# Kernel tuning notes

Measured on AMD Instinct MI355X. Metric: run time of the kernel, lower is better.

The kernel has to match this reference:

```python
import jax, jax.numpy as jnp
import numpy as np

N, K, C_IN, C = 64, 64, 128, 128


def setup_inputs() -> dict:
    key = jax.random.key(0)
    ks = jax.random.split(key, 12)
    s_in = 1.0 / np.sqrt(C_IN + 1)
    s_c = 1.0 / np.sqrt(C)
    s_2c = 1.0 / np.sqrt(2 * C)
    return {
        "t": jax.random.uniform(ks[0], (1,), dtype=jnp.float32),
        "x": jax.random.normal(ks[1], (N, K, C_IN), dtype=jnp.float32),
        # ConcatLinear: Linear(C_IN + 1, C) applied to cat([x, t], -1)
        "W_lin": jax.random.normal(ks[2], (C, C_IN + 1), dtype=jnp.float32) * s_in,
        "b_lin": jax.random.normal(ks[3], (C,), dtype=jnp.float32) * s_in,
        # unary_passing: Linear(C,C) -> tanh -> Linear(C,C)
        "Wu1": jax.random.normal(ks[4], (C, C), dtype=jnp.float32) * s_c,
        "bu1": jax.random.normal(ks[5], (C,), dtype=jnp.float32) * s_c,
        "Wu2": jax.random.normal(ks[6], (C, C), dtype=jnp.float32) * s_c,
        "bu2": jax.random.normal(ks[7], (C,), dtype=jnp.float32) * s_c,
        # binary_passing: Linear(2C,C) -> tanh -> Linear(C,C)
        "Wb1": jax.random.normal(ks[8], (C, 2 * C), dtype=jnp.float32) * s_2c,
        "bb1": jax.random.normal(ks[9], (C,), dtype=jnp.float32) * s_2c,
        "Wb2": jax.random.normal(ks[10], (C, C), dtype=jnp.float32) * s_c,
        "bb2": jax.random.normal(ks[11], (C,), dtype=jnp.float32) * s_c,
    }


def reference(t, x, W_lin, b_lin, Wu1, bu1, Wu2, bu2, Wb1, bb1, Wb2, bb2):
    n, k, _ = x.shape
    # linear_map: ConcatLinear(t, x) = Linear(cat([x, t*ones], -1))
    tt = jnp.broadcast_to(t.reshape(1, 1, 1), (n, k, 1)).astype(x.dtype)
    h = jnp.concatenate([x, tt], axis=-1) @ W_lin.T + b_lin  # [N,K,C]

    # unary message
    unary = jnp.tanh(h @ Wu1.T + bu1) @ Wu2.T + bu2  # [N,K,C]

    # binary message. h_matrix[n,i,j] = cat([h[n,j], h[n,i]]); split Wb1 into
    # the halves acting on each part to avoid materializing the 2C concat.
    A = h @ Wb1[:, :C].T          # contribution of h[n,j], [N,K,C]
    B = h @ Wb1[:, C:].T          # contribution of h[n,i], [N,K,C]
    pre = A[:, None, :, :] + B[:, :, None, :] + bb1       # [N,i,j,C]
    msg = jnp.tanh(pre) @ Wb2.T + bb2                     # [N,i,j,C]

    # fully-connected graph: E[i,j] = 1 - eye (E is None, masks is None)
    E = 1.0 - jnp.eye(k, dtype=x.dtype)                   # [i,j]
    msg = msg * E[None, :, :, None]
    denom = 1.0 + jnp.sum(E, axis=0)                      # per-j, [K]
    binary = jnp.sum(msg, axis=1) / denom[None, :, None]  # [N,K,C]

    return unary + binary
```

## Files before the change

kernel.cpp:

```cpp
#include <hip/hip_runtime.h>

#define LS 132
#define USTR 20
#define ROW_ELEMS 524288
#define EXPC 2.8853900817779268f

__device__ __forceinline__ float sigterm(float x) {
    float e = __builtin_amdgcn_exp2f(x * EXPC);
    return __builtin_amdgcn_rcpf(e + 1.0f);
}
__device__ __forceinline__ float tanh_fast(float x) {
    return 1.0f - 2.0f * sigterm(x);
}

__device__ __forceinline__ void stage64(const float* __restrict__ X, int r0,
                                        float* __restrict__ xs, int tid) {
    const float4* src = reinterpret_cast<const float4*>(X + (size_t)r0 * 128);
#pragma unroll
    for (int p = 0; p < 8; ++p) {
        const int q = p * 256 + tid;
        const int r = q >> 5;
        const int k4 = (q & 31) << 2;
        *reinterpret_cast<float4*>(&xs[r * LS + k4]) = src[q];
    }
}

template <int NC>
__device__ __forceinline__ void accum_lds(const float* __restrict__ xs,
                                          const float* __restrict__ wt,
                                          int lane, int wc0,
                                          float (&acc)[NC]) {
#pragma unroll 8
    for (int kq = 0; kq < 32; ++kq) {
        const float4 a =
            *reinterpret_cast<const float4*>(&xs[lane * LS + kq * 4]);
#pragma unroll
        for (int c = 0; c < NC; ++c) {
            const float4 w = *reinterpret_cast<const float4*>(
                &wt[(wc0 + c) * 128 + kq * 4]);
            acc[c] = fmaf(a.x, w.x, acc[c]);
            acc[c] = fmaf(a.y, w.y, acc[c]);
            acc[c] = fmaf(a.z, w.z, acc[c]);
            acc[c] = fmaf(a.w, w.w, acc[c]);
        }
    }
}

__global__ __launch_bounds__(256) void k1_h(const float* __restrict__ x,
                                            const float* __restrict__ W_lin,
                                            const float* __restrict__ b_lin,
                                            const float* __restrict__ tp,
                                            float* __restrict__ h) {
    __shared__ float xs[64 * LS];
    const int tid = threadIdx.x;
    const int lane = tid & 63;
    const int wv = __builtin_amdgcn_readfirstlane(tid >> 6);
    const int r0 = blockIdx.x * 64;
    const int c0 = blockIdx.y * 8 + wv * 2;
    stage64(x, r0, xs, tid);
    __syncthreads();
    float acc[2] = {0.f, 0.f};
    const float* w0 = W_lin + (c0 + 0) * 129;
    const float* w1 = W_lin + (c0 + 1) * 129;
#pragma unroll 8
    for (int kq = 0; kq < 32; ++kq) {
        const float4 a =
            *reinterpret_cast<const float4*>(&xs[lane * LS + kq * 4]);
        acc[0] = fmaf(a.x, w0[kq * 4 + 0], acc[0]);
        acc[0] = fmaf(a.y, w0[kq * 4 + 1], acc[0]);
        acc[0] = fmaf(a.z, w0[kq * 4 + 2], acc[0]);
        acc[0] = fmaf(a.w, w0[kq * 4 + 3], acc[0]);
        acc[1] = fmaf(a.x, w1[kq * 4 + 0], acc[1]);
        acc[1] = fmaf(a.y, w1[kq * 4 + 1], acc[1]);
        acc[1] = fmaf(a.z, w1[kq * 4 + 2], acc[1]);
        acc[1] = fmaf(a.w, w1[kq * 4 + 3], acc[1]);
    }
    const float tv = tp[0];
    float2 o;
    o.x = acc[0] + b_lin[c0 + 0] + tv * W_lin[(c0 + 0) * 129 + 128];
    o.y = acc[1] + b_lin[c0 + 1] + tv * W_lin[(c0 + 1) * 129 + 128];
    *reinterpret_cast<float2*>(&h[(size_t)(r0 + lane) * 128 + c0]) = o;
}

__global__ __launch_bounds__(256) void k2_fused(
    const float* __restrict__ h, const float* __restrict__ Wu1,
    const float* __restrict__ bu1, const float* __restrict__ Wb1,
    const float* __restrict__ bb1, float* __restrict__ T,
    float* __restrict__ S) {
    __shared__ float smem[64 * LS + 32 * 128];
    float* xs = smem;
    float* wt = smem + 64 * LS;
    float* us = smem;
    float* vs = smem + 64 * USTR;
    const int tid = threadIdx.x;
    const int lane = tid & 63;
    const int wv = __builtin_amdgcn_readfirstlane(tid >> 6);
    const int r0 = blockIdx.x * 64;
    const int j = blockIdx.y;
    stage64(h, r0, xs, tid);
    {
        const int cb = j < 8 ? j * 16 : 0;
        const int cg0 = j >= 8 ? (j - 8) * 32 : 0;
#pragma unroll
        for (int p = 0; p < 4; ++p) {
            const int q = p * 256 + tid;
            const int row = q >> 5;
            const int k4 = (q & 31) << 2;
            const float* src;
            if (j < 8)
                src = (row < 16) ? (Wb1 + (cb + row) * 256 + k4)
                                 : (Wb1 + (cb + row - 16) * 256 + 128 + k4);
            else
                src = Wu1 + (cg0 + row) * 128 + k4;
            *reinterpret_cast<float4*>(&wt[row * 128 + k4]) =
                *reinterpret_cast<const float4*>(src);
        }
    }
    __syncthreads();

    if (j < 8) {
        const int cb = j * 16;
        const bool isB = wv >= 2;
        const int half = wv & 1;
        const int c0 = cb + half * 8;
        const int wc0 = (isB ? 16 : 0) + half * 8;
        float acc[8] = {0.f, 0.f, 0.f, 0.f, 0.f, 0.f, 0.f, 0.f};
        accum_lds<8>(xs, wt, lane, wc0, acc);
        float e[8];
#pragma unroll
        for (int c = 0; c < 8; ++c) {
            const float v = isB ? (acc[c] + bb1[c0 + c]) : acc[c];
            e[c] = __builtin_amdgcn_exp2f(v * EXPC);
        }
        __syncthreads();
        float* dstl = (isB ? vs : us) + lane * USTR + half * 8;
        *reinterpret_cast<float4*>(dstl) = make_float4(e[0], e[1], e[2], e[3]);
        *reinterpret_cast<float4*>(dstl + 4) =
            make_float4(e[4], e[5], e[6], e[7]);
        __syncthreads();

        const int lc = wv * 4;
        const float4 u =
            *reinterpret_cast<const float4*>(&us[lane * USTR + lc]);
        float s0 = 0.f, s1 = 0.f, s2 = 0.f, s3 = 0.f;
#pragma unroll 8
        for (int i = 0; i < 64; ++i) {
            const float4 v =
                *reinterpret_cast<const float4*>(&vs[i * USTR + lc]);
            s0 += __builtin_amdgcn_rcpf(fmaf(u.x, v.x, 1.0f));
            s1 += __builtin_amdgcn_rcpf(fmaf(u.y, v.y, 1.0f));
            s2 += __builtin_amdgcn_rcpf(fmaf(u.z, v.z, 1.0f));
            s3 += __builtin_amdgcn_rcpf(fmaf(u.w, v.w, 1.0f));
        }
        const float4 vj =
            *reinterpret_cast<const float4*>(&vs[lane * USTR + lc]);
        float4 o;
        o.x = (63.0f - 2.0f * (s0 - __builtin_amdgcn_rcpf(fmaf(u.x, vj.x, 1.0f)))) * 0.015625f;
        o.y = (63.0f - 2.0f * (s1 - __builtin_amdgcn_rcpf(fmaf(u.y, vj.y, 1.0f)))) * 0.015625f;
        o.z = (63.0f - 2.0f * (s2 - __builtin_amdgcn_rcpf(fmaf(u.z, vj.z, 1.0f)))) * 0.015625f;
        o.w = (63.0f - 2.0f * (s3 - __builtin_amdgcn_rcpf(fmaf(u.w, vj.w, 1.0f)))) * 0.015625f;
        *reinterpret_cast<float4*>(&S[(size_t)(r0 + lane) * 128 + cb + lc]) = o;
    } else {
        const int c0 = (j - 8) * 32 + wv * 8;
        float acc[8] = {0.f, 0.f, 0.f, 0.f, 0.f, 0.f, 0.f, 0.f};
        accum_lds<8>(xs, wt, lane, wv * 8, acc);
        float4 v0, v1;
        v0.x = tanh_fast(acc[0] + bu1[c0 + 0]);
        v0.y = tanh_fast(acc[1] + bu1[c0 + 1]);
        v0.z = tanh_fast(acc[2] + bu1[c0 + 2]);
        v0.w = tanh_fast(acc[3] + bu1[c0 + 3]);
        v1.x = tanh_fast(acc[4] + bu1[c0 + 4]);
        v1.y = tanh_fast(acc[5] + bu1[c0 + 5]);
        v1.z = tanh_fast(acc[6] + bu1[c0 + 6]);
        v1.w = tanh_fast(acc[7] + bu1[c0 + 7]);
        float* dst = T + (size_t)(r0 + lane) * 128 + c0;
        *reinterpret_cast<float4*>(dst) = v0;
        *reinterpret_cast<float4*>(dst + 4) = v1;
    }
}

__global__ __launch_bounds__(256) void k4_out(
    const float* __restrict__ T, const float* __restrict__ S,
    const float* __restrict__ Wu2, const float* __restrict__ Wb2,
    const float* __restrict__ bu2, const float* __restrict__ bb2,
    float* __restrict__ out) {
    __shared__ float xs[64 * LS];
    const int tid = threadIdx.x;
    const int lane = tid & 63;
    const int wv = __builtin_amdgcn_readfirstlane(tid >> 6);
    const int r0 = blockIdx.x * 64;
    const int c0 = blockIdx.y * 8 + wv * 2;
    stage64(T, r0, xs, tid);
    __syncthreads();
    float acc[2] = {0.f, 0.f};
    {
        const float* w0 = Wu2 + (c0 + 0) * 128;
        const float* w1 = Wu2 + (c0 + 1) * 128;
#pragma unroll 8
        for (int kq = 0; kq < 32; ++kq) {
            const float4 a =
                *reinterpret_cast<const float4*>(&xs[lane * LS + kq * 4]);
            acc[0] = fmaf(a.x, w0[kq * 4 + 0], acc[0]);
            acc[0] = fmaf(a.y, w0[kq * 4 + 1], acc[0]);
            acc[0] = fmaf(a.z, w0[kq * 4 + 2], acc[0]);
            acc[0] = fmaf(a.w, w0[kq * 4 + 3], acc[0]);
            acc[1] = fmaf(a.x, w1[kq * 4 + 0], acc[1]);
            acc[1] = fmaf(a.y, w1[kq * 4 + 1], acc[1]);
            acc[1] = fmaf(a.z, w1[kq * 4 + 2], acc[1]);
            acc[1] = fmaf(a.w, w1[kq * 4 + 3], acc[1]);
        }
    }
    __syncthreads();
    stage64(S, r0, xs, tid);
    __syncthreads();
    {
        const float* w0 = Wb2 + (c0 + 0) * 128;
        const float* w1 = Wb2 + (c0 + 1) * 128;
#pragma unroll 8
        for (int kq = 0; kq < 32; ++kq) {
            const float4 a =
                *reinterpret_cast<const float4*>(&xs[lane * LS + kq * 4]);
            acc[0] = fmaf(a.x, w0[kq * 4 + 0], acc[0]);
            acc[0] = fmaf(a.y, w0[kq * 4 + 1], acc[0]);
            acc[0] = fmaf(a.z, w0[kq * 4 + 2], acc[0]);
            acc[0] = fmaf(a.w, w0[kq * 4 + 3], acc[0]);
            acc[1] = fmaf(a.x, w1[kq * 4 + 0], acc[1]);
            acc[1] = fmaf(a.y, w1[kq * 4 + 1], acc[1]);
            acc[1] = fmaf(a.z, w1[kq * 4 + 2], acc[1]);
            acc[1] = fmaf(a.w, w1[kq * 4 + 3], acc[1]);
        }
    }
    float2 o;
    o.x = acc[0] + bu2[c0 + 0] + 0.984375f * bb2[c0 + 0];
    o.y = acc[1] + bu2[c0 + 1] + 0.984375f * bb2[c0 + 1];
    *reinterpret_cast<float2*>(&out[(size_t)(r0 + lane) * 128 + c0]) = o;
}

extern "C" void kernel_launch(void* const* d_in, const int* in_sizes, int n_in,
                              void* d_out, int out_size, void* d_ws,
                              size_t ws_size, hipStream_t stream) {
    const float* t = (const float*)d_in[0];
    const float* x = (const float*)d_in[1];
    const float* W_lin = (const float*)d_in[2];
    const float* b_lin = (const float*)d_in[3];
    const float* Wu1 = (const float*)d_in[4];
    const float* bu1 = (const float*)d_in[5];
    const float* Wu2 = (const float*)d_in[6];
    const float* bu2 = (const float*)d_in[7];
    const float* Wb1 = (const float*)d_in[8];
    const float* bb1 = (const float*)d_in[9];
    const float* Wb2 = (const float*)d_in[10];
    const float* bb2 = (const float*)d_in[11];
    float* out = (float*)d_out;

    float* ws = (float*)d_ws;
    float* h = ws;
    float* T = ws + 1 * ROW_ELEMS;
    float* S = ws + 2 * ROW_ELEMS;

    k1_h<<<dim3(64, 16), 256, 0, stream>>>(x, W_lin, b_lin, t, h);
    k2_fused<<<dim3(64, 12), 256, 0, stream>>>(h, Wu1, bu1, Wb1, bb1, T, S);
    k4_out<<<dim3(64, 16), 256, 0, stream>>>(T, S, Wu2, Wb2, bu2, bb2, out);
    (void)in_sizes; (void)n_in; (void)out_size; (void)ws_size;
}
```

Before: 32.80 us.

## Merge three kernels into one persistent megakernel with per-group atomic counters

Replaces the three launches (h projection, fused first layers, output layers) with one 64x12-block kernel. Blocks coordinate through per-row-group atomic counters with release/acquire spin-waits, so later stages start as soon as their rows are ready. The next stage's weights are staged into LDS before waiting. This removes two launch gaps and kernel-boundary drains, but adds a memset launch and spin-wait overhead. It also relies on all dependent blocks being co-resident to avoid deadlock.

```diff
diff --git a/kernel.cpp b/kernel.cpp
--- a/kernel.cpp
+++ b/kernel.cpp
@@ -5,12 +5,9 @@
 #define ROW_ELEMS 524288
 #define EXPC 2.8853900817779268f
 
-__device__ __forceinline__ float sigterm(float x) {
+__device__ __forceinline__ float tanh_fast(float x) {
     float e = __builtin_amdgcn_exp2f(x * EXPC);
-    return __builtin_amdgcn_rcpf(e + 1.0f);
-}
-__device__ __forceinline__ float tanh_fast(float x) {
-    return 1.0f - 2.0f * sigterm(x);
+    return 1.0f - 2.0f * __builtin_amdgcn_rcpf(e + 1.0f);
 }
 
 __device__ __forceinline__ void stage64(const float* __restrict__ X, int r0,
@@ -46,47 +43,15 @@
     }
 }
 
-__global__ __launch_bounds__(256) void k1_h(const float* __restrict__ x,
-                                            const float* __restrict__ W_lin,
-                                            const float* __restrict__ b_lin,
-                                            const float* __restrict__ tp,
-                                            float* __restrict__ h) {
-    __shared__ float xs[64 * LS];
-    const int tid = threadIdx.x;
-    const int lane = tid & 63;
-    const int wv = __builtin_amdgcn_readfirstlane(tid >> 6);
-    const int r0 = blockIdx.x * 64;
-    const int c0 = blockIdx.y * 8 + wv * 2;
-    stage64(x, r0, xs, tid);
-    __syncthreads();
-    float acc[2] = {0.f, 0.f};
-    const float* w0 = W_lin + (c0 + 0) * 129;
-    const float* w1 = W_lin + (c0 + 1) * 129;
-#pragma unroll 8
-    for (int kq = 0; kq < 32; ++kq) {
-        const float4 a =
-            *reinterpret_cast<const float4*>(&xs[lane * LS + kq * 4]);
-        acc[0] = fmaf(a.x, w0[kq * 4 + 0], acc[0]);
-        acc[0] = fmaf(a.y, w0[kq * 4 + 1], acc[0]);
-        acc[0] = fmaf(a.z, w0[kq * 4 + 2], acc[0]);
-        acc[0] = fmaf(a.w, w0[kq * 4 + 3], acc[0]);
-        acc[1] = fmaf(a.x, w1[kq * 4 + 0], acc[1]);
-        acc[1] = fmaf(a.y, w1[kq * 4 + 1], acc[1]);
-        acc[1] = fmaf(a.z, w1[kq * 4 + 2], acc[1]);
-        acc[1] = fmaf(a.w, w1[kq * 4 + 3], acc[1]);
-    }
-    const float tv = tp[0];
-    float2 o;
-    o.x = acc[0] + b_lin[c0 + 0] + tv * W_lin[(c0 + 0) * 129 + 128];
-    o.y = acc[1] + b_lin[c0 + 1] + tv * W_lin[(c0 + 1) * 129 + 128];
-    *reinterpret_cast<float2*>(&h[(size_t)(r0 + lane) * 128 + c0]) = o;
-}
-
-__global__ __launch_bounds__(256) void k2_fused(
-    const float* __restrict__ h, const float* __restrict__ Wu1,
-    const float* __restrict__ bu1, const float* __restrict__ Wb1,
-    const float* __restrict__ bb1, float* __restrict__ T,
-    float* __restrict__ S) {
+__global__ __launch_bounds__(256) void megakernel(
+    const float* __restrict__ tp, const float* __restrict__ x,
+    const float* __restrict__ W_lin, const float* __restrict__ b_lin,
+    const float* __restrict__ Wu1, const float* __restrict__ bu1,
+    const float* __restrict__ Wu2, const float* __restrict__ bu2,
+    const float* __restrict__ Wb1, const float* __restrict__ bb1,
+    const float* __restrict__ Wb2, const float* __restrict__ bb2,
+    float* __restrict__ h, float* __restrict__ T, float* __restrict__ S,
+    float* __restrict__ out, unsigned int* __restrict__ cnt) {
     __shared__ float smem[64 * LS + 32 * 128];
     float* xs = smem;
     float* wt = smem + 64 * LS;
@@ -95,9 +60,38 @@
     const int tid = threadIdx.x;
     const int lane = tid & 63;
     const int wv = __builtin_amdgcn_readfirstlane(tid >> 6);
-    const int r0 = blockIdx.x * 64;
+    const int g = blockIdx.x;
     const int j = blockIdx.y;
-    stage64(h, r0, xs, tid);
+    const int r0 = g * 64;
+    unsigned int* c1 = cnt + g;
+    unsigned int* c2 = cnt + 64 + g;
+
+    if (j < 8) {
+        stage64(x, r0, xs, tid);
+#pragma unroll
+        for (int p = 0; p < 8; ++p) {
+            const int q = p * 256 + tid;
+            const int row = q >> 7;
+            const int col = q & 127;
+            wt[row * 128 + col] = W_lin[(j * 16 + row) * 129 + col];
+        }
+        __syncthreads();
+        float acc[4] = {0.f, 0.f, 0.f, 0.f};
+        accum_lds<4>(xs, wt, lane, wv * 4, acc);
+        const int c0 = j * 16 + wv * 4;
+        const float tv = tp[0];
+        float4 o;
+        o.x = acc[0] + b_lin[c0 + 0] + tv * W_lin[(c0 + 0) * 129 + 128];
+        o.y = acc[1] + b_lin[c0 + 1] + tv * W_lin[(c0 + 1) * 129 + 128];
+        o.z = acc[2] + b_lin[c0 + 2] + tv * W_lin[(c0 + 2) * 129 + 128];
+        o.w = acc[3] + b_lin[c0 + 3] + tv * W_lin[(c0 + 3) * 129 + 128];
+        *reinterpret_cast<float4*>(&h[(size_t)(r0 + lane) * 128 + c0]) = o;
+        __syncthreads();
+        if (tid == 0)
+            __hip_atomic_fetch_add(c1, 1u, __ATOMIC_RELEASE,
+                                   __HIP_MEMORY_SCOPE_AGENT);
+    }
+
     {
         const int cb = j < 8 ? j * 16 : 0;
         const int cg0 = j >= 8 ? (j - 8) * 32 : 0;
@@ -116,6 +110,13 @@
                 *reinterpret_cast<const float4*>(src);
         }
     }
+    if (tid == 0) {
+        while (__hip_atomic_load(c1, __ATOMIC_ACQUIRE,
+                                 __HIP_MEMORY_SCOPE_AGENT) < 8u)
+            __builtin_amdgcn_s_sleep(1);
+    }
+    __syncthreads();
+    stage64(h, r0, xs, tid);
     __syncthreads();
 
     if (j < 8) {
@@ -177,63 +178,46 @@
         *reinterpret_cast<float4*>(dst) = v0;
         *reinterpret_cast<float4*>(dst + 4) = v1;
     }
-}
-
-__global__ __launch_bounds__(256) void k4_out(
-    const float* __restrict__ T, const float* __restrict__ S,
-    const float* __restrict__ Wu2, const float* __restrict__ Wb2,
-    const float* __restrict__ bu2, const float* __restrict__ bb2,
-    float* __restrict__ out) {
-    __shared__ float xs[64 * LS];
-    const int tid = threadIdx.x;
-    const int lane = tid & 63;
-    const int wv = __builtin_amdgcn_readfirstlane(tid >> 6);
-    const int r0 = blockIdx.x * 64;
-    const int c0 = blockIdx.y * 8 + wv * 2;
-    stage64(T, r0, xs, tid);
     __syncthreads();
-    float acc[2] = {0.f, 0.f};
-    {
-        const float* w0 = Wu2 + (c0 + 0) * 128;
-        const float* w1 = Wu2 + (c0 + 1) * 128;
-#pragma unroll 8
-        for (int kq = 0; kq < 32; ++kq) {
-            const float4 a =
-                *reinterpret_cast<const float4*>(&xs[lane * LS + kq * 4]);
-            acc[0] = fmaf(a.x, w0[kq * 4 + 0], acc[0]);
-            acc[0] = fmaf(a.y, w0[kq * 4 + 1], acc[0]);
-            acc[0] = fmaf(a.z, w0[kq * 4 + 2], acc[0]);
-            acc[0] = fmaf(a.w, w0[kq * 4 + 3], acc[0]);
-            acc[1] = fmaf(a.x, w1[kq * 4 + 0], acc[1]);
-            acc[1] = fmaf(a.y, w1[kq * 4 + 1], acc[1]);
-            acc[1] = fmaf(a.z, w1[kq * 4 + 2], acc[1]);
-            acc[1] = fmaf(a.w, w1[kq * 4 + 3], acc[1]);
-        }
-    }
-    __syncthreads();
-    stage64(S, r0, xs, tid);
-    __syncthreads();
-    {
-        const float* w0 = Wb2 + (c0 + 0) * 128;
-        const float* w1 = Wb2 + (c0 + 1) * 128;
-#pragma unroll 8
-        for (int kq = 0; kq < 32; ++kq) {
-            const float4 a =
-                *reinterpret_cast<const float4*>(&xs[lane * LS + kq * 4]);
-            acc[0] = fmaf(a.x, w0[kq * 4 + 0], acc[0]);
-            acc[0] = fmaf(a.y, w0[kq * 4 + 1], acc[0]);
-            acc[0] = fmaf(a.z, w0[kq * 4 + 2], acc[0]);
-            acc[0] = fmaf(a.w, w0[kq * 4 + 3], acc[0]);
-            acc[1] = fmaf(a.x, w1[kq * 4 + 0], acc[1]);
-            acc[1] = fmaf(a.y, w1[kq * 4 + 1], acc[1]);
-            acc[1] = fmaf(a.z, w1[kq * 4 + 2], acc[1]);
-            acc[1] = fmaf(a.w, w1[kq * 4 + 3], acc[1]);
-        }
-    }
-    float2 o;
-    o.x = acc[0] + bu2[c0 + 0] + 0.984375f * bb2[c0 + 0];
-    o.y = acc[1] + bu2[c0 + 1] + 0.984375f * bb2[c0 + 1];
-    *reinterpret_cast<float2*>(&out[(size_t)(r0 + lane) * 128 + c0]) = o;
+    if (tid == 0)
+        __hip_atomic_fetch_add(c2, 1u, __ATOMIC_RELEASE,
+                               __HIP_MEMORY_SCOPE_AGENT);
+
+    if (j < 8) {
+        const int cb = j * 16;
+#pragma unroll
+        for (int p = 0; p < 4; ++p) {
+            const int q = p * 256 + tid;
+            const int row = q >> 5;
+            const int k4 = (q & 31) << 2;
+            const float* src = (row < 16)
+                                   ? (Wu2 + (cb + row) * 128 + k4)
+                                   : (Wb2 + (cb + row - 16) * 128 + k4);
+            *reinterpret_cast<float4*>(&wt[row * 128 + k4]) =
+                *reinterpret_cast<const float4*>(src);
+        }
+        if (tid == 0) {
+            while (__hip_atomic_load(c2, __ATOMIC_ACQUIRE,
+                                     __HIP_MEMORY_SCOPE_AGENT) < 12u)
+                __builtin_amdgcn_s_sleep(1);
+        }
+        __syncthreads();
+        stage64(T, r0, xs, tid);
+        __syncthreads();
+        float acc[4] = {0.f, 0.f, 0.f, 0.f};
+        accum_lds<4>(xs, wt, lane, wv * 4, acc);
+        __syncthreads();
+        stage64(S, r0, xs, tid);
+        __syncthreads();
+        accum_lds<4>(xs, wt, lane, 16 + wv * 4, acc);
+        const int c0 = cb + wv * 4;
+        float4 o;
+        o.x = acc[0] + bu2[c0 + 0] + 0.984375f * bb2[c0 + 0];
+        o.y = acc[1] + bu2[c0 + 1] + 0.984375f * bb2[c0 + 1];
+        o.z = acc[2] + bu2[c0 + 2] + 0.984375f * bb2[c0 + 2];
+        o.w = acc[3] + bu2[c0 + 3] + 0.984375f * bb2[c0 + 3];
+        *reinterpret_cast<float4*>(&out[(size_t)(r0 + lane) * 128 + c0]) = o;
+    }
 }
 
 extern "C" void kernel_launch(void* const* d_in, const int* in_sizes, int n_in,
@@ -257,9 +241,11 @@
     float* h = ws;
     float* T = ws + 1 * ROW_ELEMS;
     float* S = ws + 2 * ROW_ELEMS;
-
-    k1_h<<<dim3(64, 16), 256, 0, stream>>>(x, W_lin, b_lin, t, h);
-    k2_fused<<<dim3(64, 12), 256, 0, stream>>>(h, Wu1, bu1, Wb1, bb1, T, S);
-    k4_out<<<dim3(64, 16), 256, 0, stream>>>(T, S, Wu2, Wb2, bu2, bb2, out);
+    unsigned int* cnt = (unsigned int*)(ws + 3 * ROW_ELEMS);
+
+    hipMemsetAsync(cnt, 0, 128 * sizeof(unsigned int), stream);
+    megakernel<<<dim3(64, 12), 256, 0, stream>>>(
+        t, x, W_lin, b_lin, Wu1, bu1, Wu2, bu2, Wb1, bb1, Wb2, bb2, h, T, S,
+        out, cnt);
     (void)in_sizes; (void)n_in; (void)out_size; (void)ws_size;
 }
```

Result: slower. 101.3 us (+209.0%).

## Fold ConcatLinear weights into downstream layer weights, skipping h materialization

Applied to the files above, without the earlier changes.

Replaces the per-row h = Linear(cat(x,t)) kernel with a small kernel that precomputes composed weights Wu1·W_lin, Wb1a·W_lin, Wb1b·W_lin and composed biases that include the t term. The fused kernel then reads x directly, which removes the write and re-read of the 4096x128 h buffer. The composition kernel does 3x128x128x128 MACs on weights in every call, and reassociating the matmul changes floating-point rounding slightly.

```diff
diff --git a/kernel.cpp b/kernel.cpp
--- a/kernel.cpp
+++ b/kernel.cpp
@@ -5,12 +5,9 @@
 #define ROW_ELEMS 524288
 #define EXPC 2.8853900817779268f
 
-__device__ __forceinline__ float sigterm(float x) {
+__device__ __forceinline__ float tanh_fast(float x) {
     float e = __builtin_amdgcn_exp2f(x * EXPC);
-    return __builtin_amdgcn_rcpf(e + 1.0f);
-}
-__device__ __forceinline__ float tanh_fast(float x) {
-    return 1.0f - 2.0f * sigterm(x);
+    return 1.0f - 2.0f * __builtin_amdgcn_rcpf(e + 1.0f);
 }
 
 __device__ __forceinline__ void stage64(const float* __restrict__ X, int r0,
@@ -46,58 +43,71 @@
     }
 }
 
-__global__ __launch_bounds__(256) void k1_h(const float* __restrict__ x,
-                                            const float* __restrict__ W_lin,
-                                            const float* __restrict__ b_lin,
-                                            const float* __restrict__ tp,
-                                            float* __restrict__ h) {
-    __shared__ float xs[64 * LS];
+__global__ __launch_bounds__(256) void k0_comp(
+    const float* __restrict__ W_lin, const float* __restrict__ b_lin,
+    const float* __restrict__ Wu1, const float* __restrict__ bu1,
+    const float* __restrict__ Wb1, const float* __restrict__ bb1,
+    const float* __restrict__ tp, float* __restrict__ Wc,
+    float* __restrict__ bias) {
     const int tid = threadIdx.x;
     const int lane = tid & 63;
     const int wv = __builtin_amdgcn_readfirstlane(tid >> 6);
-    const int r0 = blockIdx.x * 64;
-    const int c0 = blockIdx.y * 8 + wv * 2;
-    stage64(x, r0, xs, tid);
-    __syncthreads();
-    float acc[2] = {0.f, 0.f};
-    const float* w0 = W_lin + (c0 + 0) * 129;
-    const float* w1 = W_lin + (c0 + 1) * 129;
-#pragma unroll 8
-    for (int kq = 0; kq < 32; ++kq) {
-        const float4 a =
-            *reinterpret_cast<const float4*>(&xs[lane * LS + kq * 4]);
-        acc[0] = fmaf(a.x, w0[kq * 4 + 0], acc[0]);
-        acc[0] = fmaf(a.y, w0[kq * 4 + 1], acc[0]);
-        acc[0] = fmaf(a.z, w0[kq * 4 + 2], acc[0]);
-        acc[0] = fmaf(a.w, w0[kq * 4 + 3], acc[0]);
-        acc[1] = fmaf(a.x, w1[kq * 4 + 0], acc[1]);
-        acc[1] = fmaf(a.y, w1[kq * 4 + 1], acc[1]);
-        acc[1] = fmaf(a.z, w1[kq * 4 + 2], acc[1]);
-        acc[1] = fmaf(a.w, w1[kq * 4 + 3], acc[1]);
-    }
+    const int bid = blockIdx.x;
+    const int comp = bid >> 5;
+    const int r = (bid & 31) * 4 + wv;
+    const float* w2;
+    if (comp == 0)
+        w2 = Wu1 + r * 128;
+    else if (comp == 1)
+        w2 = Wb1 + r * 256;
+    else
+        w2 = Wb1 + r * 256 + 128;
+
+    float a0 = 0.f, a1 = 0.f;
+#pragma unroll 8
+    for (int e = 0; e < 128; ++e) {
+        const float w2e = w2[e];
+        a0 = fmaf(w2e, W_lin[e * 129 + lane], a0);
+        a1 = fmaf(w2e, W_lin[e * 129 + lane + 64], a1);
+    }
+    Wc[comp * 16384 + r * 128 + lane] = a0;
+    Wc[comp * 16384 + r * 128 + lane + 64] = a1;
+
     const float tv = tp[0];
-    float2 o;
-    o.x = acc[0] + b_lin[c0 + 0] + tv * W_lin[(c0 + 0) * 129 + 128];
-    o.y = acc[1] + b_lin[c0 + 1] + tv * W_lin[(c0 + 1) * 129 + 128];
-    *reinterpret_cast<float2*>(&h[(size_t)(r0 + lane) * 128 + c0]) = o;
+    const float hb0 = b_lin[lane] + tv * W_lin[lane * 129 + 128];
+    const float hb1 = b_lin[lane + 64] + tv * W_lin[(lane + 64) * 129 + 128];
+    float pb = w2[lane] * hb0 + w2[lane + 64] * hb1;
+#pragma unroll
+    for (int m = 32; m >= 1; m >>= 1) pb += __shfl_xor(pb, m, 64);
+    if (lane == 0) {
+        float base = 0.f;
+        if (comp == 0) base = bu1[r];
+        else if (comp == 2) base = bb1[r];
+        bias[comp * 128 + r] = pb + base;
+    }
 }
 
 __global__ __launch_bounds__(256) void k2_fused(
-    const float* __restrict__ h, const float* __restrict__ Wu1,
-    const float* __restrict__ bu1, const float* __restrict__ Wb1,
-    const float* __restrict__ bb1, float* __restrict__ T,
+    const float* __restrict__ x, const float* __restrict__ Wc,
+    const float* __restrict__ bias, float* __restrict__ T,
     float* __restrict__ S) {
     __shared__ float smem[64 * LS + 32 * 128];
     float* xs = smem;
     float* wt = smem + 64 * LS;
     float* us = smem;
     float* vs = smem + 64 * USTR;
+    const float* WcU = Wc;
+    const float* WcA = Wc + 16384;
+    const float* WcB = Wc + 32768;
+    const float* bU = bias;
+    const float* bA = bias + 128;
+    const float* bB = bias + 256;
     const int tid = threadIdx.x;
     const int lane = tid & 63;
     const int wv = __builtin_amdgcn_readfirstlane(tid >> 6);
     const int r0 = blockIdx.x * 64;
     const int j = blockIdx.y;
-    stage64(h, r0, xs, tid);
+    stage64(x, r0, xs, tid);
     {
         const int cb = j < 8 ? j * 16 : 0;
         const int cg0 = j >= 8 ? (j - 8) * 32 : 0;
@@ -108,10 +118,10 @@
             const int k4 = (q & 31) << 2;
             const float* src;
             if (j < 8)
-                src = (row < 16) ? (Wb1 + (cb + row) * 256 + k4)
-                                 : (Wb1 + (cb + row - 16) * 256 + 128 + k4);
+                src = (row < 16) ? (WcA + (cb + row) * 128 + k4)
+                                 : (WcB + (cb + row - 16) * 128 + k4);
             else
-                src = Wu1 + (cg0 + row) * 128 + k4;
+                src = WcU + (cg0 + row) * 128 + k4;
             *reinterpret_cast<float4*>(&wt[row * 128 + k4]) =
                 *reinterpret_cast<const float4*>(src);
         }
@@ -129,7 +139,7 @@
         float e[8];
 #pragma unroll
         for (int c = 0; c < 8; ++c) {
-            const float v = isB ? (acc[c] + bb1[c0 + c]) : acc[c];
+            const float v = acc[c] + (isB ? bB[c0 + c] : bA[c0 + c]);
             e[c] = __builtin_amdgcn_exp2f(v * EXPC);
         }
         __syncthreads();
@@ -165,14 +175,14 @@
         float acc[8] = {0.f, 0.f, 0.f, 0.f, 0.f, 0.f, 0.f, 0.f};
         accum_lds<8>(xs, wt, lane, wv * 8, acc);
         float4 v0, v1;
-        v0.x = tanh_fast(acc[0] + bu1[c0 + 0]);
-        v0.y = tanh_fast(acc[1] + bu1[c0 + 1]);
-        v0.z = tanh_fast(acc[2] + bu1[c0 + 2]);
-        v0.w = tanh_fast(acc[3] + bu1[c0 + 3]);
-        v1.x = tanh_fast(acc[4] + bu1[c0 + 4]);
-        v1.y = tanh_fast(acc[5] + bu1[c0 + 5]);
-        v1.z = tanh_fast(acc[6] + bu1[c0 + 6]);
-        v1.w = tanh_fast(acc[7] + bu1[c0 + 7]);
+        v0.x = tanh_fast(acc[0] + bU[c0 + 0]);
+        v0.y = tanh_fast(acc[1] + bU[c0 + 1]);
+        v0.z = tanh_fast(acc[2] + bU[c0 + 2]);
+        v0.w = tanh_fast(acc[3] + bU[c0 + 3]);
+        v1.x = tanh_fast(acc[4] + bU[c0 + 4]);
+        v1.y = tanh_fast(acc[5] + bU[c0 + 5]);
+        v1.z = tanh_fast(acc[6] + bU[c0 + 6]);
+        v1.w = tanh_fast(acc[7] + bU[c0 + 7]);
         float* dst = T + (size_t)(r0 + lane) * 128 + c0;
         *reinterpret_cast<float4*>(dst) = v0;
         *reinterpret_cast<float4*>(dst + 4) = v1;
@@ -254,12 +264,14 @@
     float* out = (float*)d_out;
 
     float* ws = (float*)d_ws;
-    float* h = ws;
+    float* Wc = ws;
+    float* bias = ws + 49152;
     float* T = ws + 1 * ROW_ELEMS;
     float* S = ws + 2 * ROW_ELEMS;
 
-    k1_h<<<dim3(64, 16), 256, 0, stream>>>(x, W_lin, b_lin, t, h);
-    k2_fused<<<dim3(64, 12), 256, 0, stream>>>(h, Wu1, bu1, Wb1, bb1, T, S);
+    k0_comp<<<96, 256, 0, stream>>>(W_lin, b_lin, Wu1, bu1, Wb1, bb1, t, Wc,
+                                    bias);
+    k2_fused<<<dim3(64, 12), 256, 0, stream>>>(x, Wc, bias, T, S);
     k4_out<<<dim3(64, 16), 256, 0, stream>>>(T, S, Wu2, Wb2, bu2, bb2, out);
     (void)in_sizes; (void)n_in; (void)out_size; (void)ws_size;
 }
```

Result: slower. 33.51 us (+2.2%).
